# Performance work log

Measured on AMD Instinct MI355X. Metric: run time of the kernel, lower is better.

The kernel has to match this reference:

```python
import jax, jax.numpy as jnp
import numpy as np

B, S, HID = 1, 2048, 3072
NH, NKV, HD = 24, 8, 128
ROT = 96
OP = NH * HD + 2 * NKV * HD
MASK_VALUE = -jnp.finfo(jnp.float32).max


def setup_inputs() -> dict:
    key = jax.random.key(0)
    k1, k2, k3, k4, k5 = jax.random.split(key, 5)
    hidden_states = jax.random.normal(k1, (B, S, HID), dtype=jnp.float32)
    # rotary embeddings: use actual cos/sin of rope angles for realism
    inv_freq = 1.0 / (10000.0 ** (jnp.arange(0, ROT, 2, dtype=jnp.float32) / ROT))
    t = jnp.arange(S, dtype=jnp.float32)
    freqs = jnp.outer(t, inv_freq)  # [S, ROT/2]
    emb = jnp.concatenate([freqs, freqs], axis=-1)  # [S, ROT]
    cos = jnp.broadcast_to(jnp.cos(emb)[None], (B, S, ROT))
    sin = jnp.broadcast_to(jnp.sin(emb)[None], (B, S, ROT))
    attention_mask = jnp.ones((B, S), dtype=bool)
    w_qkv = jax.random.normal(k2, (OP, HID), dtype=jnp.float32) * (HID ** -0.5)
    w_o = jax.random.normal(k3, (HID, HID), dtype=jnp.float32) * (HID ** -0.5)
    return {"hidden_states": hidden_states, "cos": cos, "sin": sin,
            "attention_mask": attention_mask, "w_qkv": w_qkv, "w_o": w_o}


def rotate_half(x):
    x1, x2 = jnp.split(x, 2, axis=-1)
    return jnp.concatenate([-x2, x1], axis=-1)


def apply_rope(q, k, cos, sin):
    # cos/sin: [B, S, ROT] -> [B, 1, S, ROT]
    cos = cos[:, None]
    sin = sin[:, None]
    rd = cos.shape[-1]
    q_rot, q_pass = q[..., :rd], q[..., rd:]
    k_rot, k_pass = k[..., :rd], k[..., rd:]
    q = jnp.concatenate([q_rot * cos + rotate_half(q_rot) * sin, q_pass], axis=-1)
    k = jnp.concatenate([k_rot * cos + rotate_half(k_rot) * sin, k_pass], axis=-1)
    return q, k


def reference(hidden_states, cos, sin, attention_mask, w_qkv, w_o):
    b, n, _ = hidden_states.shape
    qkv = hidden_states @ w_qkv.T  # [B, S, OP]
    q, k, v = jnp.split(qkv, [NH * HD, NH * HD + NKV * HD], axis=-1)
    # b n (h d) -> b h n d
    q = q.reshape(b, n, NH, HD).transpose(0, 2, 1, 3)
    k = k.reshape(b, n, NKV, HD).transpose(0, 2, 1, 3)
    v = v.reshape(b, n, NKV, HD).transpose(0, 2, 1, 3)
    q, k = apply_rope(q, k, cos, sin)
    q = q * (HD ** -0.5)
    n_rep = NH // NKV
    if n_rep > 1:
        k = jnp.repeat(k, n_rep, axis=1)
        v = jnp.repeat(v, n_rep, axis=1)
    sim = jnp.einsum('bhid,bhjd->bhij', q, k)
    causal = jnp.triu(jnp.ones((n, n), dtype=bool), k=1)
    sim = jnp.where(causal, MASK_VALUE, sim)
    sim = jnp.where(~attention_mask[:, None, None, :], MASK_VALUE, sim)
    attn = jax.nn.softmax(sim.astype(jnp.float32), axis=-1).astype(v.dtype)
    out = jnp.einsum('bhij,bhjd->bhid', attn, v)
    out = out.transpose(0, 2, 1, 3).reshape(b, n, NH * HD)  # b h n d -> b n (h d)
    return out @ w_o.T
```

## Files before the change

kernel.cpp:

```cpp
#include <hip/hip_runtime.h>

typedef unsigned short u16;
typedef unsigned int u32;
typedef __bf16 bf16x8 __attribute__((ext_vector_type(8)));
typedef float f32x4 __attribute__((ext_vector_type(4)));

#define S_LEN 2048
#define HIDDEN 3072
#define NHEADS 24
#define NKVH 8
#define HDIM 128
#define QKVW 5120
#define QKLD 4096
#define PSTR 80

__device__ __forceinline__ u16 f2bf(float f) {
  u32 u = __float_as_uint(f);
  u32 r = (u + 0x7fffu + ((u >> 16) & 1u)) >> 16;
  return (u16)r;
}
__device__ __forceinline__ float bf2f(u16 h) { return __uint_as_float(((u32)h) << 16); }

__device__ __forceinline__ void gload_lds16(const void* g, void* l) {
  __builtin_amdgcn_global_load_lds((const __attribute__((address_space(1))) void*)g,
                                   (__attribute__((address_space(3))) void*)l, 16, 0, 0);
}

__global__ void cast4(const float4* __restrict__ in, uint2* __restrict__ out, int n4) {
  int i = blockIdx.x * blockDim.x + threadIdx.x;
  if (i >= n4) return;
  float4 f = in[i];
  uint2 o;
  o.x = ((u32)f2bf(f.y) << 16) | f2bf(f.x);
  o.y = ((u32)f2bf(f.w) << 16) | f2bf(f.z);
  out[i] = o;
}

template <bool OUT_BF16, bool WRITE_VT>
__global__ __launch_bounds__(256) void gemm_bt(const u16* __restrict__ A, const u16* __restrict__ B,
                                               float* __restrict__ Cf, u16* __restrict__ Cb,
                                               u16* __restrict__ vtg,
                                               int M, int N, int K, int ldc) {
  __shared__ u16 As[128 * 32];
  __shared__ u16 Bs[128 * 32];
  const int tid = threadIdx.x;
  const int w = tid >> 6, lane = tid & 63;
  const int wm = w & 1, wn = w >> 1;
  const int l15 = lane & 15, qd = lane >> 4;
  const int m0 = blockIdx.y * 128, n0 = blockIdx.x * 128;
  const int rS = lane >> 2, cS = (lane & 3) * 8;
  f32x4 acc[4][4] = {};
  for (int k0 = 0; k0 < K; k0 += 32) {
    __syncthreads();
#pragma unroll
    for (int t = 0; t < 2; ++t) {
      int r = t * 64 + w * 16;
      gload_lds16(A + (size_t)(m0 + r + rS) * K + k0 + cS, &As[r * 32]);
      gload_lds16(B + (size_t)(n0 + r + rS) * K + k0 + cS, &Bs[r * 32]);
    }
    __syncthreads();
    bf16x8 af[4], bfm[4];
#pragma unroll
    for (int i = 0; i < 4; ++i) af[i] = *(const bf16x8*)&As[(wm * 64 + i * 16 + l15) * 32 + qd * 8];
#pragma unroll
    for (int j = 0; j < 4; ++j) bfm[j] = *(const bf16x8*)&Bs[(wn * 64 + j * 16 + l15) * 32 + qd * 8];
#pragma unroll
    for (int i = 0; i < 4; ++i)
#pragma unroll
      for (int j = 0; j < 4; ++j)
        acc[i][j] = __builtin_amdgcn_mfma_f32_16x16x32_bf16(af[i], bfm[j], acc[i][j], 0, 0, 0);
  }
  if (WRITE_VT && n0 >= 4096) {
#pragma unroll
    for (int i = 0; i < 4; ++i)
#pragma unroll
      for (int j = 0; j < 4; ++j) {
        int n = (n0 - 4096) + wn * 64 + j * 16 + l15;
        int m = m0 + wm * 64 + i * 16 + qd * 4;
        uint2 p;
        p.x = ((u32)f2bf(acc[i][j][1]) << 16) | f2bf(acc[i][j][0]);
        p.y = ((u32)f2bf(acc[i][j][3]) << 16) | f2bf(acc[i][j][2]);
        *(uint2*)&vtg[(size_t)n * S_LEN + m] = p;
      }
    return;
  }
#pragma unroll
  for (int i = 0; i < 4; ++i)
#pragma unroll
    for (int j = 0; j < 4; ++j)
#pragma unroll
      for (int r = 0; r < 4; ++r) {
        int m = m0 + wm * 64 + i * 16 + qd * 4 + r;
        int n = n0 + wn * 64 + j * 16 + l15;
        if (OUT_BF16) Cb[(size_t)m * ldc + n] = f2bf(acc[i][j][r]);
        else          Cf[(size_t)m * ldc + n] = acc[i][j][r];
      }
}

template <bool OUT_BF16>
__global__ __launch_bounds__(256) void gemm_bt64(const u16* __restrict__ A, const u16* __restrict__ B,
                                                 float* __restrict__ Cf, u16* __restrict__ Cb,
                                                 int M, int N, int K, int ldc) {
  __shared__ u16 As[64 * 32];
  __shared__ u16 Bs[128 * 32];
  const int tid = threadIdx.x;
  const int w = tid >> 6, lane = tid & 63;
  const int wm = w & 1, wn = w >> 1;
  const int l15 = lane & 15, qd = lane >> 4;
  const int m0 = blockIdx.y * 64, n0 = blockIdx.x * 128;
  const int rS = lane >> 2, cS = (lane & 3) * 8;
  f32x4 acc[2][4] = {};
  for (int k0 = 0; k0 < K; k0 += 32) {
    __syncthreads();
    gload_lds16(A + (size_t)(m0 + w * 16 + rS) * K + k0 + cS, &As[w * 16 * 32]);
#pragma unroll
    for (int t = 0; t < 2; ++t) {
      int r = t * 64 + w * 16;
      gload_lds16(B + (size_t)(n0 + r + rS) * K + k0 + cS, &Bs[r * 32]);
    }
    __syncthreads();
    bf16x8 af[2], bfm[4];
#pragma unroll
    for (int i = 0; i < 2; ++i) af[i] = *(const bf16x8*)&As[(wm * 32 + i * 16 + l15) * 32 + qd * 8];
#pragma unroll
    for (int j = 0; j < 4; ++j) bfm[j] = *(const bf16x8*)&Bs[(wn * 64 + j * 16 + l15) * 32 + qd * 8];
#pragma unroll
    for (int i = 0; i < 2; ++i)
#pragma unroll
      for (int j = 0; j < 4; ++j)
        acc[i][j] = __builtin_amdgcn_mfma_f32_16x16x32_bf16(af[i], bfm[j], acc[i][j], 0, 0, 0);
  }
#pragma unroll
  for (int i = 0; i < 2; ++i)
#pragma unroll
    for (int j = 0; j < 4; ++j)
#pragma unroll
      for (int r = 0; r < 4; ++r) {
        int m = m0 + wm * 32 + i * 16 + qd * 4 + r;
        int n = n0 + wn * 64 + j * 16 + l15;
        if (OUT_BF16) Cb[(size_t)m * ldc + n] = f2bf(acc[i][j][r]);
        else          Cf[(size_t)m * ldc + n] = acc[i][j][r];
      }
}

__global__ __launch_bounds__(128) void rope_kernel(u16* __restrict__ qkv,
                                                   const float* __restrict__ cosb,
                                                   const float* __restrict__ sinb) {
  const int s = blockIdx.x;
  const int hh = blockIdx.y;
  const int d = threadIdx.x;
  const bool isq = hh < NHEADS;
  const size_t base = (size_t)s * QKLD + (isq ? hh * HDIM : HIDDEN + (hh - NHEADS) * HDIM);
  const float scale = 0.08838834764831845f;
  if (d < 48) {
    float x1 = bf2f(qkv[base + d]), x2 = bf2f(qkv[base + d + 48]);
    float c1 = cosb[s * 96 + d], s1 = sinb[s * 96 + d];
    float c2 = cosb[s * 96 + d + 48], s2 = sinb[s * 96 + d + 48];
    float o1 = x1 * c1 - x2 * s1;
    float o2 = x2 * c2 + x1 * s2;
    if (isq) { o1 *= scale; o2 *= scale; }
    qkv[base + d] = f2bf(o1);
    qkv[base + d + 48] = f2bf(o2);
  } else if (d >= 96 && isq) {
    qkv[base + d] = f2bf(bf2f(qkv[base + d]) * scale);
  }
}

__global__ __launch_bounds__(256) void flash_kernel(const u16* __restrict__ qkv,
                                                    const u16* __restrict__ vtg,
                                                    u16* __restrict__ ao) {
  __shared__ u16 Ks[4][64 * 32];
  __shared__ u16 Vt[128 * PSTR];
  __shared__ u16 Ps[64 * PSTR];
  const int bid = blockIdx.x;
  const int g = bid & 255, kk3 = bid >> 8;
  const int rank = (kk3 == 1) ? (kk3 << 8) + (255 - g) : (kk3 << 8) + g;
  const int h = rank % NHEADS;
  const int qi = 31 - rank / NHEADS;
  const int q0 = qi * 64;
  const int hkv = h / 3;
  const int tid = threadIdx.x;
  const int w = tid >> 6, lane = tid & 63;
  const int l15 = lane & 15, qd = lane >> 4;
  const int rS = lane >> 2, cS = (lane & 3) * 8;

  bf16x8 qf[4];
#pragma unroll
  for (int kk = 0; kk < 4; ++kk)
    qf[kk] = *(const bf16x8*)&qkv[(size_t)(q0 + w * 16 + l15) * QKLD + h * HDIM + kk * 32 + qd * 8];

  f32x4 o[8] = {};
  float lrow[4] = {0.f, 0.f, 0.f, 0.f};

  const u16* vb = vtg + (size_t)hkv * HDIM * S_LEN;
  const int vd = tid >> 3;
  const int vkv = (tid & 7) * 8;

  for (int kv0 = 0; kv0 <= q0; kv0 += 64) {
    __syncthreads();
#pragma unroll
    for (int t = 0; t < 4; ++t)
      gload_lds16(qkv + (size_t)(kv0 + t * 16 + rS) * QKLD + HIDDEN + hkv * HDIM + w * 32 + cS,
                  &Ks[w][t * 16 * 32]);
#pragma unroll
    for (int it = 0; it < 4; ++it) {
      int d = it * 32 + vd;
      uint4 vv = *(const uint4*)&vb[(size_t)d * S_LEN + kv0 + vkv];
      *(uint4*)&Vt[d * PSTR + vkv] = vv;
    }
    __syncthreads();

    f32x4 sc[4] = {};
#pragma unroll
    for (int j = 0; j < 4; ++j)
#pragma unroll
      for (int kk = 0; kk < 4; ++kk) {
        bf16x8 kf = *(const bf16x8*)&Ks[kk][(j * 16 + l15) * 32 + qd * 8];
        sc[j] = __builtin_amdgcn_mfma_f32_16x16x32_bf16(qf[kk], kf, sc[j], 0, 0, 0);
      }

    if (kv0 == q0) {
#pragma unroll
      for (int j = 0; j < 4; ++j)
#pragma unroll
        for (int r = 0; r < 4; ++r) {
          int row = w * 16 + qd * 4 + r;
          int col = j * 16 + l15;
          if (col > row) sc[j][r] = -1.0e30f;
        }
    }

#pragma unroll
    for (int j = 0; j < 4; ++j)
#pragma unroll
      for (int r = 0; r < 4; ++r) sc[j][r] = __expf(sc[j][r]);
#pragma unroll
    for (int r = 0; r < 4; ++r)
      lrow[r] += (sc[0][r] + sc[1][r]) + (sc[2][r] + sc[3][r]);

#pragma unroll
    for (int j = 0; j < 4; ++j)
#pragma unroll
      for (int r = 0; r < 4; ++r)
        Ps[(w * 16 + qd * 4 + r) * PSTR + j * 16 + l15] = f2bf(sc[j][r]);
    asm volatile("s_waitcnt lgkmcnt(0)" ::: "memory");

    bf16x8 pf[2];
#pragma unroll
    for (int kk = 0; kk < 2; ++kk)
      pf[kk] = *(const bf16x8*)&Ps[(w * 16 + l15) * PSTR + kk * 32 + qd * 8];
#pragma unroll
    for (int jn = 0; jn < 8; ++jn)
#pragma unroll
      for (int kk = 0; kk < 2; ++kk) {
        bf16x8 vf = *(const bf16x8*)&Vt[(jn * 16 + l15) * PSTR + kk * 32 + qd * 8];
        o[jn] = __builtin_amdgcn_mfma_f32_16x16x32_bf16(pf[kk], vf, o[jn], 0, 0, 0);
      }
  }

  float rinv[4];
#pragma unroll
  for (int r = 0; r < 4; ++r) {
    float s = lrow[r];
#pragma unroll
    for (int d = 1; d < 16; d <<= 1) s += __shfl_xor(s, d, 64);
    rinv[r] = 1.0f / s;
  }
#pragma unroll
  for (int jn = 0; jn < 8; ++jn)
#pragma unroll
    for (int r = 0; r < 4; ++r) {
      int row = q0 + w * 16 + qd * 4 + r;
      ao[(size_t)row * HIDDEN + h * HDIM + jn * 16 + l15] = f2bf(o[jn][r] * rinv[r]);
    }
}

extern "C" void kernel_launch(void* const* d_in, const int* in_sizes, int n_in,
                              void* d_out, int out_size, void* d_ws, size_t ws_size,
                              hipStream_t stream) {
  (void)in_sizes; (void)n_in; (void)out_size; (void)ws_size;
  const float* hs   = (const float*)d_in[0];
  const float* cosb = (const float*)d_in[1];
  const float* sinb = (const float*)d_in[2];
  const float* wqkv = (const float*)d_in[4];
  const float* wo   = (const float*)d_in[5];
  float* out = (float*)d_out;
  char* ws = (char*)d_ws;

  u16* hB   = (u16*)ws;
  u16* wB   = (u16*)(ws + 12582912);
  u16* qkvB = (u16*)(ws + 44040192);
  u16* vtgB = (u16*)(ws + 60817408);
  u16* aoB  = hB;
  u16* woB  = wB;

  cast4<<<6144, 256, 0, stream>>>((const float4*)hs, (uint2*)hB, 1572864);
  cast4<<<15360, 256, 0, stream>>>((const float4*)wqkv, (uint2*)wB, 3932160);
  gemm_bt<true, true><<<dim3(40, 16), 256, 0, stream>>>(hB, wB, nullptr, qkvB, vtgB,
                                                        2048, QKVW, 3072, QKLD);
  cast4<<<9216, 256, 0, stream>>>((const float4*)wo, (uint2*)woB, 2359296);
  rope_kernel<<<dim3(2048, 32), 128, 0, stream>>>(qkvB, cosb, sinb);
  flash_kernel<<<768, 256, 0, stream>>>(qkvB, vtgB, aoB);
  gemm_bt64<false><<<dim3(24, 32), 256, 0, stream>>>(aoB, woB, out, nullptr,
                                                     2048, HIDDEN, 3072, HIDDEN);
}
```

Baseline: 404.1 us.

## Rewrite QKV GEMM with 256x256 tiles, 4-stage LDS pipeline and swizzle

Replaces the 128x128 single-buffered QKV projection GEMM with a 256x256-tile, 512-thread kernel. It prefetches K-slices three stages ahead into a 4-deep LDS ring, uses an XOR-swizzled LDS layout to avoid bank conflicts, and remaps block indices for L2 locality. MFMA sections are wrapped in s_setprio. The goal is to hide global-load latency and raise data reuse per tile. The trade-offs are only 160 blocks, which may underfill the 256 CUs, and heavy LDS and register use.

```diff
diff --git a/kernel.cpp b/kernel.cpp
--- a/kernel.cpp
+++ b/kernel.cpp
@@ -36,64 +36,125 @@
   out[i] = o;
 }
 
-template <bool OUT_BF16, bool WRITE_VT>
-__global__ __launch_bounds__(256) void gemm_bt(const u16* __restrict__ A, const u16* __restrict__ B,
-                                               float* __restrict__ Cf, u16* __restrict__ Cb,
-                                               u16* __restrict__ vtg,
-                                               int M, int N, int K, int ldc) {
-  __shared__ u16 As[128 * 32];
-  __shared__ u16 Bs[128 * 32];
+__global__ __launch_bounds__(512, 2) void gemm256(const u16* __restrict__ A,
+                                                  const u16* __restrict__ B,
+                                                  u16* __restrict__ Cb,
+                                                  u16* __restrict__ vtg) {
+  __shared__ u16 lds[4][2][8192];
   const int tid = threadIdx.x;
   const int w = tid >> 6, lane = tid & 63;
-  const int wm = w & 1, wn = w >> 1;
+  const int wm = w >> 2, wn = w & 3;
   const int l15 = lane & 15, qd = lane >> 4;
-  const int m0 = blockIdx.y * 128, n0 = blockIdx.x * 128;
-  const int rS = lane >> 2, cS = (lane & 3) * 8;
-  f32x4 acc[4][4] = {};
-  for (int k0 = 0; k0 < K; k0 += 32) {
-    __syncthreads();
-#pragma unroll
-    for (int t = 0; t < 2; ++t) {
-      int r = t * 64 + w * 16;
-      gload_lds16(A + (size_t)(m0 + r + rS) * K + k0 + cS, &As[r * 32]);
-      gload_lds16(B + (size_t)(n0 + r + rS) * K + k0 + cS, &Bs[r * 32]);
-    }
-    __syncthreads();
-    bf16x8 af[4], bfm[4];
-#pragma unroll
-    for (int i = 0; i < 4; ++i) af[i] = *(const bf16x8*)&As[(wm * 64 + i * 16 + l15) * 32 + qd * 8];
-#pragma unroll
-    for (int j = 0; j < 4; ++j) bfm[j] = *(const bf16x8*)&Bs[(wn * 64 + j * 16 + l15) * 32 + qd * 8];
+  const int K = 3072;
+  const int swz = (blockIdx.x & 7) * 20 + (blockIdx.x >> 3);
+  const int n0 = (swz % 20) * 256;
+  const int m0 = (swz / 20) * 256;
+
+  size_t offA[2], offB[2];
+  int ldsU[2];
+#pragma unroll
+  for (int it = 0; it < 2; ++it) {
+    int CH = (w * 2 + it) * 64 + lane;
+    int rp = CH >> 3, sl = CH & 7;
+    int lin = sl ^ (rp & 7);
+    int r = (rp << 1) | (lin >> 2), q = lin & 3;
+    offA[it] = (size_t)(m0 + r) * K + q * 8;
+    offB[it] = (size_t)(n0 + r) * K + q * 8;
+    ldsU[it] = (w * 2 + it) * 512;
+  }
+
+  int chA[8], chB[4];
+#pragma unroll
+  for (int i = 0; i < 8; ++i) {
+    int r = wm * 128 + i * 16 + l15;
+    chA[i] = (r >> 1) * 8 + ((((r & 1) << 2) | qd) ^ ((r >> 1) & 7));
+  }
+#pragma unroll
+  for (int j = 0; j < 4; ++j) {
+    int r = wn * 64 + j * 16 + l15;
+    chB[j] = (r >> 1) * 8 + ((((r & 1) << 2) | qd) ^ ((r >> 1) & 7));
+  }
+
+  f32x4 acc[8][4] = {};
+
+  auto stage = [&](int s, int k0, int ab) {
+    const u16* src = ab ? B : A;
+    const size_t* off = ab ? offB : offA;
+#pragma unroll
+    for (int it = 0; it < 2; ++it)
+      gload_lds16(src + off[it] + k0, &lds[s][ab][ldsU[it]]);
+  };
+
+  auto tile = [&](int s, int spf, int kpf, bool pf) {
+    bf16x8 a[4], bq[4];
+    if (pf) stage(spf, kpf, 0);
+#pragma unroll
+    for (int i = 0; i < 4; ++i) a[i] = *(const bf16x8*)&lds[s][0][chA[i] << 3];
+#pragma unroll
+    for (int j = 0; j < 4; ++j) bq[j] = *(const bf16x8*)&lds[s][1][chB[j] << 3];
+    __builtin_amdgcn_s_setprio(1);
 #pragma unroll
     for (int i = 0; i < 4; ++i)
 #pragma unroll
       for (int j = 0; j < 4; ++j)
-        acc[i][j] = __builtin_amdgcn_mfma_f32_16x16x32_bf16(af[i], bfm[j], acc[i][j], 0, 0, 0);
-  }
-  if (WRITE_VT && n0 >= 4096) {
+        acc[i][j] = __builtin_amdgcn_mfma_f32_16x16x32_bf16(a[i], bq[j], acc[i][j], 0, 0, 0);
+    __builtin_amdgcn_s_setprio(0);
+    __builtin_amdgcn_s_barrier();
+    if (pf) stage(spf, kpf, 1);
+#pragma unroll
+    for (int i = 0; i < 4; ++i) a[i] = *(const bf16x8*)&lds[s][0][chA[i + 4] << 3];
+    __builtin_amdgcn_s_setprio(1);
 #pragma unroll
     for (int i = 0; i < 4; ++i)
 #pragma unroll
+      for (int j = 0; j < 4; ++j)
+        acc[i + 4][j] = __builtin_amdgcn_mfma_f32_16x16x32_bf16(a[i], bq[j], acc[i + 4][j], 0, 0, 0);
+    __builtin_amdgcn_s_setprio(0);
+  };
+
+  stage(0, 0, 0);  stage(0, 0, 1);
+  stage(1, 32, 0); stage(1, 32, 1);
+  stage(2, 64, 0); stage(2, 64, 1);
+  asm volatile("s_waitcnt vmcnt(8)" ::: "memory");
+  __builtin_amdgcn_s_barrier();
+
+  const int NT = 96;
+  for (int t = 0; t < NT - 3; ++t) {
+    tile(t & 3, (t + 3) & 3, (t + 3) * 32, true);
+    asm volatile("s_waitcnt vmcnt(8)" ::: "memory");
+    __builtin_amdgcn_s_barrier();
+  }
+  tile(1, 0, 0, false);
+  asm volatile("s_waitcnt vmcnt(4)" ::: "memory");
+  __builtin_amdgcn_s_barrier();
+  tile(2, 0, 0, false);
+  asm volatile("s_waitcnt vmcnt(0)" ::: "memory");
+  __builtin_amdgcn_s_barrier();
+  tile(3, 0, 0, false);
+
+  if (n0 >= 4096) {
+#pragma unroll
+    for (int i = 0; i < 8; ++i)
+#pragma unroll
       for (int j = 0; j < 4; ++j) {
-        int n = (n0 - 4096) + wn * 64 + j * 16 + l15;
-        int m = m0 + wm * 64 + i * 16 + qd * 4;
+        int nv = n0 - 4096 + wn * 64 + j * 16 + l15;
+        int m = m0 + wm * 128 + i * 16 + qd * 4;
         uint2 p;
         p.x = ((u32)f2bf(acc[i][j][1]) << 16) | f2bf(acc[i][j][0]);
         p.y = ((u32)f2bf(acc[i][j][3]) << 16) | f2bf(acc[i][j][2]);
-        *(uint2*)&vtg[(size_t)n * S_LEN + m] = p;
+        *(uint2*)&vtg[(size_t)nv * S_LEN + m] = p;
       }
     return;
   }
 #pragma unroll
-  for (int i = 0; i < 4; ++i)
+  for (int i = 0; i < 8; ++i)
 #pragma unroll
     for (int j = 0; j < 4; ++j)
 #pragma unroll
       for (int r = 0; r < 4; ++r) {
-        int m = m0 + wm * 64 + i * 16 + qd * 4 + r;
+        int m = m0 + wm * 128 + i * 16 + qd * 4 + r;
         int n = n0 + wn * 64 + j * 16 + l15;
-        if (OUT_BF16) Cb[(size_t)m * ldc + n] = f2bf(acc[i][j][r]);
-        else          Cf[(size_t)m * ldc + n] = acc[i][j][r];
+        Cb[(size_t)m * QKLD + n] = f2bf(acc[i][j][r]);
       }
 }
 
@@ -296,8 +357,7 @@
 
   cast4<<<6144, 256, 0, stream>>>((const float4*)hs, (uint2*)hB, 1572864);
   cast4<<<15360, 256, 0, stream>>>((const float4*)wqkv, (uint2*)wB, 3932160);
-  gemm_bt<true, true><<<dim3(40, 16), 256, 0, stream>>>(hB, wB, nullptr, qkvB, vtgB,
-                                                        2048, QKVW, 3072, QKLD);
+  gemm256<<<160, 512, 0, stream>>>(hB, wB, qkvB, vtgB);
   cast4<<<9216, 256, 0, stream>>>((const float4*)wo, (uint2*)woB, 2359296);
   rope_kernel<<<dim3(2048, 32), 128, 0, stream>>>(qkvB, cosb, sinb);
   flash_kernel<<<768, 256, 0, stream>>>(qkvB, vtgB, aoB);
```

Result: no change. 397.2 us (-1.7%).

## Replace QKV GEMM with 256x160 tile, 4-stage LDS pipeline and swizzled layout

Applied to the files above, without the earlier changes.

Replaces the 128x128 single-buffered QKV projection GEMM with a 512-thread kernel. Each block computes a 256x160 tile, so 256 blocks cover the output, which matches the CU count. Global-to-LDS loads run through a 4-stage ring with explicit vmcnt waits, letting loads overlap MFMA work, and the LDS layout is XOR-swizzled to avoid bank conflicts. The change aims to remove load latency stalls and improve data reuse, at the cost of a larger LDS footprint and hardcoded shapes and wait counts that are fragile.

```diff
diff --git a/kernel.cpp b/kernel.cpp
--- a/kernel.cpp
+++ b/kernel.cpp
@@ -36,65 +36,122 @@
   out[i] = o;
 }
 
-template <bool OUT_BF16, bool WRITE_VT>
-__global__ __launch_bounds__(256) void gemm_bt(const u16* __restrict__ A, const u16* __restrict__ B,
-                                               float* __restrict__ Cf, u16* __restrict__ Cb,
-                                               u16* __restrict__ vtg,
-                                               int M, int N, int K, int ldc) {
-  __shared__ u16 As[128 * 32];
-  __shared__ u16 Bs[128 * 32];
+__global__ __launch_bounds__(512, 2) void gemm256(const u16* __restrict__ A,
+                                                  const u16* __restrict__ B,
+                                                  u16* __restrict__ Cb,
+                                                  u16* __restrict__ vtg) {
+  __shared__ u16 lds[4][13312];
   const int tid = threadIdx.x;
   const int w = tid >> 6, lane = tid & 63;
-  const int wm = w & 1, wn = w >> 1;
+  const int wm = w & 3, wn = w >> 2;
   const int l15 = lane & 15, qd = lane >> 4;
-  const int m0 = blockIdx.y * 128, n0 = blockIdx.x * 128;
-  const int rS = lane >> 2, cS = (lane & 3) * 8;
-  f32x4 acc[4][4] = {};
-  for (int k0 = 0; k0 < K; k0 += 32) {
-    __syncthreads();
-#pragma unroll
-    for (int t = 0; t < 2; ++t) {
-      int r = t * 64 + w * 16;
-      gload_lds16(A + (size_t)(m0 + r + rS) * K + k0 + cS, &As[r * 32]);
-      gload_lds16(B + (size_t)(n0 + r + rS) * K + k0 + cS, &Bs[r * 32]);
-    }
-    __syncthreads();
-    bf16x8 af[4], bfm[4];
-#pragma unroll
-    for (int i = 0; i < 4; ++i) af[i] = *(const bf16x8*)&As[(wm * 64 + i * 16 + l15) * 32 + qd * 8];
-#pragma unroll
-    for (int j = 0; j < 4; ++j) bfm[j] = *(const bf16x8*)&Bs[(wn * 64 + j * 16 + l15) * 32 + qd * 8];
+  const int K = 3072;
+  const int m0 = ((int)blockIdx.x & 7) * 256;
+  const int n0 = ((int)blockIdx.x >> 3) * 160;
+
+  size_t offA[2], offB[2];
+  int ldsA[2], ldsB[2];
+#pragma unroll
+  for (int it = 0; it < 2; ++it) {
+    int CH = w * 128 + it * 64 + lane;
+    int rp = CH >> 3, sl = CH & 7;
+    int lin = sl ^ (rp & 7);
+    int r = (rp << 1) | (lin >> 2), q = lin & 3;
+    offA[it] = (size_t)(m0 + r) * K + q * 8;
+    ldsA[it] = (w * 128 + it * 64) * 8;
+  }
+#pragma unroll
+  for (int it = 0; it < 2; ++it) {
+    int CH = it * 512 + w * 64 + lane;
+    int rp = CH >> 3, sl = CH & 7;
+    int lin = sl ^ (rp & 7);
+    int r = (rp << 1) | (lin >> 2), q = lin & 3;
+    offB[it] = (size_t)(n0 + r) * K + q * 8;
+    ldsB[it] = 8192 + (it * 512 + w * 64) * 8;
+  }
+
+  int chA[4], chB[5];
+#pragma unroll
+  for (int i = 0; i < 4; ++i) {
+    int r = wm * 64 + i * 16 + l15;
+    chA[i] = ((r >> 1) * 8 + ((((r & 1) << 2) | qd) ^ ((r >> 1) & 7))) * 8;
+  }
+#pragma unroll
+  for (int j = 0; j < 5; ++j) {
+    int r = wn * 80 + j * 16 + l15;
+    chB[j] = 8192 + ((r >> 1) * 8 + ((((r & 1) << 2) | qd) ^ ((r >> 1) & 7))) * 8;
+  }
+
+  f32x4 acc[4][5] = {};
+
+  auto stage = [&](int s, int k0) {
+    gload_lds16(A + offA[0] + k0, &lds[s][ldsA[0]]);
+    gload_lds16(A + offA[1] + k0, &lds[s][ldsA[1]]);
+    gload_lds16(B + offB[0] + k0, &lds[s][ldsB[0]]);
+    if (w < 2) gload_lds16(B + offB[1] + k0, &lds[s][ldsB[1]]);
+  };
+
+  auto tile = [&](int s, int kpf, bool pf) {
+    if (pf) stage((kpf >> 5) & 3, kpf);
+    bf16x8 a[4], b[5];
+#pragma unroll
+    for (int i = 0; i < 4; ++i) a[i] = *(const bf16x8*)&lds[s][chA[i]];
+#pragma unroll
+    for (int j = 0; j < 5; ++j) b[j] = *(const bf16x8*)&lds[s][chB[j]];
+    __builtin_amdgcn_s_setprio(1);
 #pragma unroll
     for (int i = 0; i < 4; ++i)
 #pragma unroll
-      for (int j = 0; j < 4; ++j)
-        acc[i][j] = __builtin_amdgcn_mfma_f32_16x16x32_bf16(af[i], bfm[j], acc[i][j], 0, 0, 0);
-  }
-  if (WRITE_VT && n0 >= 4096) {
-#pragma unroll
-    for (int i = 0; i < 4; ++i)
-#pragma unroll
-      for (int j = 0; j < 4; ++j) {
-        int n = (n0 - 4096) + wn * 64 + j * 16 + l15;
+      for (int j = 0; j < 5; ++j)
+        acc[i][j] = __builtin_amdgcn_mfma_f32_16x16x32_bf16(a[i], b[j], acc[i][j], 0, 0, 0);
+    __builtin_amdgcn_s_setprio(0);
+  };
+
+  stage(0, 0);
+  stage(1, 32);
+  stage(2, 64);
+  if (w < 2) asm volatile("s_waitcnt vmcnt(8)" ::: "memory");
+  else       asm volatile("s_waitcnt vmcnt(6)" ::: "memory");
+  __builtin_amdgcn_s_barrier();
+
+  for (int t = 0; t < 93; ++t) {
+    tile(t & 3, (t + 3) * 32, true);
+    if (w < 2) asm volatile("s_waitcnt vmcnt(8)" ::: "memory");
+    else       asm volatile("s_waitcnt vmcnt(6)" ::: "memory");
+    __builtin_amdgcn_s_barrier();
+  }
+  tile(1, 0, false);
+  if (w < 2) asm volatile("s_waitcnt vmcnt(4)" ::: "memory");
+  else       asm volatile("s_waitcnt vmcnt(3)" ::: "memory");
+  __builtin_amdgcn_s_barrier();
+  tile(2, 0, false);
+  asm volatile("s_waitcnt vmcnt(0)" ::: "memory");
+  __builtin_amdgcn_s_barrier();
+  tile(3, 0, false);
+
+#pragma unroll
+  for (int j = 0; j < 5; ++j) {
+    const int nf = n0 + wn * 80 + j * 16;
+    if (nf >= 4096) {
+#pragma unroll
+      for (int i = 0; i < 4; ++i) {
+        int nv = nf - 4096 + l15;
         int m = m0 + wm * 64 + i * 16 + qd * 4;
         uint2 p;
         p.x = ((u32)f2bf(acc[i][j][1]) << 16) | f2bf(acc[i][j][0]);
         p.y = ((u32)f2bf(acc[i][j][3]) << 16) | f2bf(acc[i][j][2]);
-        *(uint2*)&vtg[(size_t)n * S_LEN + m] = p;
+        *(uint2*)&vtg[(size_t)nv * S_LEN + m] = p;
       }
-    return;
-  }
-#pragma unroll
-  for (int i = 0; i < 4; ++i)
-#pragma unroll
-    for (int j = 0; j < 4; ++j)
-#pragma unroll
-      for (int r = 0; r < 4; ++r) {
-        int m = m0 + wm * 64 + i * 16 + qd * 4 + r;
-        int n = n0 + wn * 64 + j * 16 + l15;
-        if (OUT_BF16) Cb[(size_t)m * ldc + n] = f2bf(acc[i][j][r]);
-        else          Cf[(size_t)m * ldc + n] = acc[i][j][r];
-      }
+    } else {
+#pragma unroll
+      for (int i = 0; i < 4; ++i)
+#pragma unroll
+        for (int r = 0; r < 4; ++r) {
+          int m = m0 + wm * 64 + i * 16 + qd * 4 + r;
+          Cb[(size_t)m * QKLD + nf + l15] = f2bf(acc[i][j][r]);
+        }
+    }
+  }
 }
 
 template <bool OUT_BF16>
@@ -296,8 +353,7 @@
 
   cast4<<<6144, 256, 0, stream>>>((const float4*)hs, (uint2*)hB, 1572864);
   cast4<<<15360, 256, 0, stream>>>((const float4*)wqkv, (uint2*)wB, 3932160);
-  gemm_bt<true, true><<<dim3(40, 16), 256, 0, stream>>>(hB, wB, nullptr, qkvB, vtgB,
-                                                        2048, QKVW, 3072, QKLD);
+  gemm256<<<256, 512, 0, stream>>>(hB, wB, qkvB, vtgB);
   cast4<<<9216, 256, 0, stream>>>((const float4*)wo, (uint2*)woB, 2359296);
   rope_kernel<<<dim3(2048, 32), 128, 0, stream>>>(qkvB, cosb, sinb);
   flash_kernel<<<768, 256, 0, stream>>>(qkvB, vtgB, aoB);
```

Result: faster. 382.8 us (-5.3%).
